# Kernel optimization log

Hardware: AMD Instinct MI355X
Metric: run time of the kernel (lower is better)

Reference implementation:

```python
import jax, jax.numpy as jnp
import numpy as np

TAU = 1.0
ALPHA = 1.0
BETA = 0.2  # note: torch module hardcodes self.beta = 0.2 regardless of the beta arg
EPS = 1e-10


def setup_inputs() -> dict:
    key = jax.random.key(0)
    k1, k2, k3 = jax.random.split(key, 3)
    N, H = 32768, 1024
    C, d, K = 8, 128, 512  # n_codebooks, code_size, K
    hidden_state = jax.random.normal(k1, (N, H), dtype=jnp.float32)
    codes = jax.random.normal(k2, (C, d, K), dtype=jnp.float32)
    u = jax.random.uniform(k3, (N, C, K), dtype=jnp.float32)
    gumbel = -jnp.log(-jnp.log(u + EPS) + EPS)  # standard Gumbel noise
    return {"hidden_state": hidden_state, "codes": codes, "gumbel": gumbel}


def reference(hidden_state, codes, gumbel):
    N, H = hidden_state.shape
    C, d, K = codes.shape
    h = hidden_state.reshape(N, C, d)  # codebook c owns columns [c*d, (c+1)*d)

    # cosine-similarity logits: (h @ code) / ||h|| / ||code||
    logits = jnp.einsum('ncd,cdk->nck', h, codes)
    feat_norms = jnp.linalg.norm(h, axis=2, keepdims=True)        # [N, C, 1]
    code_norms = jnp.linalg.norm(codes, axis=1)                   # [C, K]
    logits = logits / feat_norms / code_norms[None, :, :]

    # gumbel-softmax with hard=True (straight-through one-hot)
    y_soft = jax.nn.softmax((logits + gumbel) / TAU, axis=-1)     # [N, C, K]
    idx = jnp.argmax(y_soft, axis=-1)                             # [N, C]
    y_hard = jax.nn.one_hot(idx, K, dtype=y_soft.dtype)
    attention = y_hard + y_soft - jax.lax.stop_gradient(y_soft)

    # quantized hidden state
    nh = jnp.einsum('nck,cdk->ncd', attention, codes)             # [N, C, d]

    # VQ commitment / codebook losses (detach == stop_gradient)
    diff_commit = jax.lax.stop_gradient(nh) - h
    diff_code = nh - jax.lax.stop_gradient(h)
    loss = BETA * jnp.sum(jnp.linalg.norm(diff_commit, axis=2)) \
         + ALPHA * jnp.sum(jnp.linalg.norm(diff_code, axis=2))

    return nh.reshape(N, H), loss
```

## Files before the change

### kernel.cpp

```cpp
#include <hip/hip_runtime.h>
#include <hip/hip_bf16.h>
#include <stdint.h>

#define NROWS 32768
#define HDIM  1024
#define CNB   8
#define DCS   128
#define KCB   512
#define ROWS_PB 128

typedef short bf16x8 __attribute__((ext_vector_type(8)));
typedef float f32x4 __attribute__((ext_vector_type(4)));

__device__ __forceinline__ unsigned f2bfu(float x) {
  union { float f; unsigned u; } v; v.f = x;
  return (v.u + 0x7fffu + ((v.u >> 16) & 1u)) >> 16;
}
__device__ __forceinline__ float bfu2f(unsigned short b) {
  union { unsigned u; float f; } v; v.u = ((unsigned)b) << 16;
  return v.f;
}
__device__ __forceinline__ void gload_lds16(const void* g, void* l) {
  __builtin_amdgcn_global_load_lds(
      (const __attribute__((address_space(1))) uint32_t*)g,
      (__attribute__((address_space(3))) uint32_t*)l, 16, 0, 0);
}

__global__ __launch_bounds__(256) void prep_kernel(
    const float* __restrict__ codes, unsigned short* __restrict__ codesB,
    float* __restrict__ cn2, float* __restrict__ rcn, float* __restrict__ loss_slot) {
  const int c = blockIdx.y;
  const int k0 = blockIdx.x * 64;
  const int t = threadIdx.x;
  const int kl = t & 63;
  const int dq = t >> 6;
  const int k = k0 + kl;
  const float* src = codes + (size_t)c * DCS * KCB + k;
  char* dstbase = (char*)codesB + (size_t)c * 131072 + (size_t)(k >> 7) * 32768 + (k & 127) * 256;
  const unsigned swzk = (unsigned)(k & 7) << 4;
  float acc = 0.f;
#pragma unroll
  for (int g = 0; g < 4; ++g) {
    unsigned short pk[8];
#pragma unroll
    for (int j = 0; j < 8; ++j) {
      int d = dq * 32 + g * 8 + j;
      float v = src[(size_t)d * KCB];
      acc += v * v;
      pk[j] = (unsigned short)f2bfu(v);
    }
    unsigned d2 = (unsigned)((dq * 32 + g * 8) * 2);
    *(uint4*)(dstbase + (d2 ^ swzk)) = *(const uint4*)pk;
  }
  __shared__ float red[256];
  red[t] = acc;
  __syncthreads();
  if (t < 64) {
    float s = red[t] + red[t + 64] + red[t + 128] + red[t + 192];
    cn2[c * KCB + k0 + t] = s;
    rcn[c * KCB + k0 + t] = rsqrtf(s);
  }
  if (blockIdx.x == 0 && c == 0 && t == 0) *loss_slot = 0.f;
}

__global__ __launch_bounds__(512, 4) void vq_kernel(
    const float* __restrict__ hidden, const float* __restrict__ gumbel,
    const unsigned short* __restrict__ codesB, const float* __restrict__ cn2g,
    const float* __restrict__ rcn, float* __restrict__ out, float* __restrict__ loss_slot) {
  const int c = blockIdx.y;
  const int nb = blockIdx.x * ROWS_PB;
  const int tid = threadIdx.x;
  const int w = tid >> 6;
  const int l = tid & 63;
  const int l15 = l & 15;
  const int l4 = l >> 4;

  __shared__ char ldsB[32768];
  __shared__ float wloss[8];

  const char* cbase = (const char*)codesB + (size_t)c * 131072;

#pragma unroll
  for (int i = 0; i < 4; ++i)
    gload_lds16(cbase + i * 8192 + tid * 16, ldsB + i * 8192 + w * 1024);

  const int nrow = nb + w * 16 + l15;
  const float* hp = hidden + (size_t)nrow * HDIM + c * DCS + l4 * 8;
  float hv[4][8];
  float hn2 = 0.f;
#pragma unroll
  for (int s = 0; s < 4; ++s) {
    f32x4 p0 = *(const f32x4*)(hp + s * 32);
    f32x4 p1 = *(const f32x4*)(hp + s * 32 + 4);
#pragma unroll
    for (int j = 0; j < 4; ++j) { hv[s][j] = p0[j]; hv[s][4 + j] = p1[j]; }
#pragma unroll
    for (int j = 0; j < 8; ++j) hn2 += hv[s][j] * hv[s][j];
  }
  hn2 += __shfl_xor(hn2, 16);
  hn2 += __shfl_xor(hn2, 32);
  const float hnorm = sqrtf(hn2);
  const float rh = hnorm > 0.f ? 1.0f / hnorm : 0.f;
  bf16x8 afr[4];
#pragma unroll
  for (int s = 0; s < 4; ++s)
#pragma unroll
    for (int j = 0; j < 8; ++j) afr[s][j] = (short)f2bfu(hv[s][j] * rh);

  const float* gbase = gumbel + ((size_t)nrow * CNB + c) * KCB + l4 * 4;
  const float* rbase = rcn + c * KCB + l4 * 4;
  const unsigned swz = (unsigned)(l15 & 7) << 4;

  float bs = -3.4e38f, ba = 0.f;
  int bk = 0;

  __syncthreads();

#pragma unroll 1
  for (int kc = 0; kc < KCB; kc += 128) {
    f32x4 acc[8];
#pragma unroll
    for (int t = 0; t < 8; ++t) acc[t] = (f32x4){0.f, 0.f, 0.f, 0.f};
#pragma unroll
    for (int t = 0; t < 8; ++t) {
      const unsigned rowbase = (unsigned)((t * 16 + l15) * 256);
#pragma unroll
      for (int s = 0; s < 4; ++s) {
        bf16x8 bfr = *(const bf16x8*)(ldsB + rowbase + (((unsigned)(s * 64 + l4 * 16)) ^ swz));
        acc[t] = __builtin_amdgcn_mfma_f32_16x16x32_bf16(bfr, afr[s], acc[t], 0, 0, 0);
      }
    }
    __syncthreads();

    if (kc + 128 < KCB) {
      const char* src = cbase + (size_t)((kc >> 7) + 1) * 32768;
#pragma unroll
      for (int i = 0; i < 4; ++i)
        gload_lds16(src + i * 8192 + tid * 16, ldsB + i * 8192 + w * 1024);
    }

#pragma unroll
    for (int t = 0; t < 8; ++t) {
      f32x4 g = *(const f32x4*)(gbase + kc + t * 16);
      f32x4 rc = *(const f32x4*)(rbase + kc + t * 16);
#pragma unroll
      for (int r = 0; r < 4; ++r) {
        const int kf = kc + t * 16 + l4 * 4 + r;
        float sc = fmaf(acc[t][r], rc[r], g[r]);
        if (sc > bs) { bs = sc; bk = kf; ba = acc[t][r]; }
      }
    }
    __syncthreads();
  }

#pragma unroll
  for (int m = 16; m <= 32; m <<= 1) {
    float os = __shfl_xor(bs, m);
    int ok = __shfl_xor(bk, m);
    float oa = __shfl_xor(ba, m);
    if (os > bs || (os == bs && ok < bk)) { bs = os; bk = ok; ba = oa; }
  }

  const float c2 = cn2g[c * KCB + bk];
  const float arg = c2 + hn2 - 2.f * (ba * hnorm);
  float lsum = (l4 == 0) ? sqrtf(fmaxf(arg, 0.f)) : 0.f;

  const char* cb = cbase + (size_t)(bk >> 7) * 32768 + (bk & 127) * 256;
  const unsigned swzk = (unsigned)(bk & 7) << 4;
  float* op = out + (size_t)nrow * HDIM + c * DCS + l4 * 32;
#pragma unroll
  for (int j = 0; j < 4; ++j) {
    unsigned d2 = (unsigned)((l4 * 32 + j * 8) * 2);
    bf16x8 cv = *(const bf16x8*)(cb + (d2 ^ swzk));
    f32x4 o0, o1;
#pragma unroll
    for (int e = 0; e < 4; ++e) {
      o0[e] = bfu2f((unsigned short)cv[e]);
      o1[e] = bfu2f((unsigned short)cv[4 + e]);
    }
    *(f32x4*)(op + j * 8) = o0;
    *(f32x4*)(op + j * 8 + 4) = o1;
  }

#pragma unroll
  for (int m = 1; m <= 32; m <<= 1) lsum += __shfl_xor(lsum, m);
  if (l == 0) wloss[w] = lsum;
  __syncthreads();
  if (tid == 0) {
    float tot = 0.f;
#pragma unroll
    for (int i = 0; i < 8; ++i) tot += wloss[i];
    atomicAdd(loss_slot, tot * 1.2f);
  }
}

extern "C" void kernel_launch(void* const* d_in, const int* in_sizes, int n_in,
                              void* d_out, int out_size, void* d_ws, size_t ws_size,
                              hipStream_t stream) {
  const float* hidden = (const float*)d_in[0];
  const float* codes  = (const float*)d_in[1];
  const float* gumbel = (const float*)d_in[2];
  float* out = (float*)d_out;
  unsigned short* codesB = (unsigned short*)d_ws;
  float* cn2 = (float*)((char*)d_ws + (size_t)CNB * 131072);
  float* rcn = cn2 + CNB * KCB;
  float* loss_slot = out + (size_t)NROWS * HDIM;

  prep_kernel<<<dim3(8, CNB), 256, 0, stream>>>(codes, codesB, cn2, rcn, loss_slot);
  vq_kernel<<<dim3(NROWS / ROWS_PB, CNB), 512, 0, stream>>>(hidden, gumbel, codesB, cn2, rcn, out, loss_slot);
}
```

Before: 225.9 us.

## Double-buffer codebook LDS, prefetch gumbel, pre-normalize codes, nontemporal IO

Pre-normalizes codes to unit norm during prep, which removes the per-logit rcn load and multiply from the main loop. The output is rescaled by the code norm at write time. The codebook LDS buffer is doubled so two chunks are staged ahead and one barrier per chunk is removed, and gumbel loads for a chunk are issued before its MFMAs. Loads and stores use nontemporal hints. The cost is doubled LDS use (64KB per block), which may cut occupancy below the 4-block launch bound, plus a bf16 rounding change on the normalized codes and the rescaled output.

```diff
diff --git a/kernel.cpp b/kernel.cpp
--- a/kernel.cpp
+++ b/kernel.cpp
@@ -28,7 +28,7 @@
 
 __global__ __launch_bounds__(256) void prep_kernel(
     const float* __restrict__ codes, unsigned short* __restrict__ codesB,
-    float* __restrict__ cn2, float* __restrict__ rcn, float* __restrict__ loss_slot) {
+    float* __restrict__ cn2, float* __restrict__ loss_slot) {
   const int c = blockIdx.y;
   const int k0 = blockIdx.x * 64;
   const int t = threadIdx.x;
@@ -36,29 +36,30 @@
   const int dq = t >> 6;
   const int k = k0 + kl;
   const float* src = codes + (size_t)c * DCS * KCB + k;
-  char* dstbase = (char*)codesB + (size_t)c * 131072 + (size_t)(k >> 7) * 32768 + (k & 127) * 256;
-  const unsigned swzk = (unsigned)(k & 7) << 4;
+  float vbuf[32];
   float acc = 0.f;
 #pragma unroll
-  for (int g = 0; g < 4; ++g) {
-    unsigned short pk[8];
-#pragma unroll
-    for (int j = 0; j < 8; ++j) {
-      int d = dq * 32 + g * 8 + j;
-      float v = src[(size_t)d * KCB];
-      acc += v * v;
-      pk[j] = (unsigned short)f2bfu(v);
-    }
-    unsigned d2 = (unsigned)((dq * 32 + g * 8) * 2);
-    *(uint4*)(dstbase + (d2 ^ swzk)) = *(const uint4*)pk;
+  for (int i = 0; i < 32; ++i) {
+    float v = src[(size_t)(dq * 32 + i) * KCB];
+    vbuf[i] = v;
+    acc += v * v;
   }
   __shared__ float red[256];
   red[t] = acc;
   __syncthreads();
-  if (t < 64) {
-    float s = red[t] + red[t + 64] + red[t + 128] + red[t + 192];
-    cn2[c * KCB + k0 + t] = s;
-    rcn[c * KCB + k0 + t] = rsqrtf(s);
+  const float s = red[kl] + red[kl + 64] + red[kl + 128] + red[kl + 192];
+  const float rn = rsqrtf(s);
+  if (t < 64) cn2[c * KCB + k0 + t] = s;
+
+  char* dstbase = (char*)codesB + (size_t)c * 131072 + (size_t)(k >> 7) * 32768 + (k & 127) * 256;
+  const unsigned swzk = (unsigned)(k & 7) << 4;
+#pragma unroll
+  for (int g = 0; g < 4; ++g) {
+    unsigned short pk[8];
+#pragma unroll
+    for (int j = 0; j < 8; ++j) pk[j] = (unsigned short)f2bfu(vbuf[g * 8 + j] * rn);
+    unsigned d2 = (unsigned)((dq * 32 + g * 8) * 2);
+    *(uint4*)(dstbase + (d2 ^ swzk)) = *(const uint4*)pk;
   }
   if (blockIdx.x == 0 && c == 0 && t == 0) *loss_slot = 0.f;
 }
@@ -66,7 +67,7 @@
 __global__ __launch_bounds__(512, 4) void vq_kernel(
     const float* __restrict__ hidden, const float* __restrict__ gumbel,
     const unsigned short* __restrict__ codesB, const float* __restrict__ cn2g,
-    const float* __restrict__ rcn, float* __restrict__ out, float* __restrict__ loss_slot) {
+    float* __restrict__ out, float* __restrict__ loss_slot) {
   const int c = blockIdx.y;
   const int nb = blockIdx.x * ROWS_PB;
   const int tid = threadIdx.x;
@@ -75,28 +76,43 @@
   const int l15 = l & 15;
   const int l4 = l >> 4;
 
-  __shared__ char ldsB[32768];
+  __shared__ char ldsB[2 * 32768];
   __shared__ float wloss[8];
 
   const char* cbase = (const char*)codesB + (size_t)c * 131072;
 
-#pragma unroll
-  for (int i = 0; i < 4; ++i)
-    gload_lds16(cbase + i * 8192 + tid * 16, ldsB + i * 8192 + w * 1024);
+#define STAGE(chunk) { \
+    const char* _s = cbase + (size_t)(chunk) * 32768; \
+    char* _d = ldsB + ((chunk) & 1) * 32768 + w * 1024; \
+    gload_lds16(_s + 0 * 8192 + tid * 16, _d + 0 * 8192); \
+    gload_lds16(_s + 1 * 8192 + tid * 16, _d + 1 * 8192); \
+    gload_lds16(_s + 2 * 8192 + tid * 16, _d + 2 * 8192); \
+    gload_lds16(_s + 3 * 8192 + tid * 16, _d + 3 * 8192); }
 
   const int nrow = nb + w * 16 + l15;
   const float* hp = hidden + (size_t)nrow * HDIM + c * DCS + l4 * 8;
+  f32x4 hr[4][2];
+#pragma unroll
+  for (int s = 0; s < 4; ++s) {
+    hr[s][0] = __builtin_nontemporal_load((const f32x4*)(hp + s * 32));
+    hr[s][1] = __builtin_nontemporal_load((const f32x4*)(hp + s * 32 + 4));
+  }
+
+  STAGE(0)
+  STAGE(1)
+
+  float hn2 = 0.f;
   float hv[4][8];
-  float hn2 = 0.f;
-#pragma unroll
-  for (int s = 0; s < 4; ++s) {
-    f32x4 p0 = *(const f32x4*)(hp + s * 32);
-    f32x4 p1 = *(const f32x4*)(hp + s * 32 + 4);
-#pragma unroll
-    for (int j = 0; j < 4; ++j) { hv[s][j] = p0[j]; hv[s][4 + j] = p1[j]; }
+#pragma unroll
+  for (int s = 0; s < 4; ++s)
+#pragma unroll
+    for (int j = 0; j < 4; ++j) {
+      hv[s][j] = hr[s][0][j]; hv[s][4 + j] = hr[s][1][j];
+    }
+#pragma unroll
+  for (int s = 0; s < 4; ++s)
 #pragma unroll
     for (int j = 0; j < 8; ++j) hn2 += hv[s][j] * hv[s][j];
-  }
   hn2 += __shfl_xor(hn2, 16);
   hn2 += __shfl_xor(hn2, 32);
   const float hnorm = sqrtf(hn2);
@@ -108,7 +124,6 @@
     for (int j = 0; j < 8; ++j) afr[s][j] = (short)f2bfu(hv[s][j] * rh);
 
   const float* gbase = gumbel + ((size_t)nrow * CNB + c) * KCB + l4 * 4;
-  const float* rbase = rcn + c * KCB + l4 * 4;
   const unsigned swz = (unsigned)(l15 & 7) << 4;
 
   float bs = -3.4e38f, ba = 0.f;
@@ -116,8 +131,16 @@
 
   __syncthreads();
 
-#pragma unroll 1
-  for (int kc = 0; kc < KCB; kc += 128) {
+#pragma unroll
+  for (int i = 0; i < 4; ++i) {
+    const int kc = i * 128;
+    const char* buf = ldsB + (i & 1) * 32768;
+
+    f32x4 garr[8];
+#pragma unroll
+    for (int t = 0; t < 8; ++t)
+      garr[t] = __builtin_nontemporal_load((const f32x4*)(gbase + kc + t * 16));
+
     f32x4 acc[8];
 #pragma unroll
     for (int t = 0; t < 8; ++t) acc[t] = (f32x4){0.f, 0.f, 0.f, 0.f};
@@ -126,31 +149,23 @@
       const unsigned rowbase = (unsigned)((t * 16 + l15) * 256);
 #pragma unroll
       for (int s = 0; s < 4; ++s) {
-        bf16x8 bfr = *(const bf16x8*)(ldsB + rowbase + (((unsigned)(s * 64 + l4 * 16)) ^ swz));
+        bf16x8 bfr = *(const bf16x8*)(buf + rowbase + (((unsigned)(s * 64 + l4 * 16)) ^ swz));
         acc[t] = __builtin_amdgcn_mfma_f32_16x16x32_bf16(bfr, afr[s], acc[t], 0, 0, 0);
       }
     }
-    __syncthreads();
-
-    if (kc + 128 < KCB) {
-      const char* src = cbase + (size_t)((kc >> 7) + 1) * 32768;
-#pragma unroll
-      for (int i = 0; i < 4; ++i)
-        gload_lds16(src + i * 8192 + tid * 16, ldsB + i * 8192 + w * 1024);
-    }
 
 #pragma unroll
     for (int t = 0; t < 8; ++t) {
-      f32x4 g = *(const f32x4*)(gbase + kc + t * 16);
-      f32x4 rc = *(const f32x4*)(rbase + kc + t * 16);
 #pragma unroll
       for (int r = 0; r < 4; ++r) {
         const int kf = kc + t * 16 + l4 * 4 + r;
-        float sc = fmaf(acc[t][r], rc[r], g[r]);
+        float sc = acc[t][r] + garr[t][r];
         if (sc > bs) { bs = sc; bk = kf; ba = acc[t][r]; }
       }
     }
+
     __syncthreads();
+    if (i < 2) STAGE(i + 2)
   }
 
 #pragma unroll
@@ -162,7 +177,8 @@
   }
 
   const float c2 = cn2g[c * KCB + bk];
-  const float arg = c2 + hn2 - 2.f * (ba * hnorm);
+  const float cn = sqrtf(c2);
+  const float arg = c2 + hn2 - 2.f * (ba * hnorm * cn);
   float lsum = (l4 == 0) ? sqrtf(fmaxf(arg, 0.f)) : 0.f;
 
   const char* cb = cbase + (size_t)(bk >> 7) * 32768 + (bk & 127) * 256;
@@ -175,11 +191,11 @@
     f32x4 o0, o1;
 #pragma unroll
     for (int e = 0; e < 4; ++e) {
-      o0[e] = bfu2f((unsigned short)cv[e]);
-      o1[e] = bfu2f((unsigned short)cv[4 + e]);
-    }
-    *(f32x4*)(op + j * 8) = o0;
-    *(f32x4*)(op + j * 8 + 4) = o1;
+      o0[e] = bfu2f((unsigned short)cv[e]) * cn;
+      o1[e] = bfu2f((unsigned short)cv[4 + e]) * cn;
+    }
+    __builtin_nontemporal_store(o0, (f32x4*)(op + j * 8));
+    __builtin_nontemporal_store(o1, (f32x4*)(op + j * 8 + 4));
   }
 
 #pragma unroll
@@ -192,6 +208,7 @@
     for (int i = 0; i < 8; ++i) tot += wloss[i];
     atomicAdd(loss_slot, tot * 1.2f);
   }
+#undef STAGE
 }
 
 extern "C" void kernel_launch(void* const* d_in, const int* in_sizes, int n_in,
@@ -203,9 +220,8 @@
   float* out = (float*)d_out;
   unsigned short* codesB = (unsigned short*)d_ws;
   float* cn2 = (float*)((char*)d_ws + (size_t)CNB * 131072);
-  float* rcn = cn2 + CNB * KCB;
   float* loss_slot = out + (size_t)NROWS * HDIM;
 
-  prep_kernel<<<dim3(8, CNB), 256, 0, stream>>>(codes, codesB, cn2, rcn, loss_slot);
-  vq_kernel<<<dim3(NROWS / ROWS_PB, CNB), 512, 0, stream>>>(hidden, gumbel, codesB, cn2, rcn, out, loss_slot);
-}
+  prep_kernel<<<dim3(8, CNB), 256, 0, stream>>>(codes, codesB, cn2, loss_slot);
+  vq_kernel<<<dim3(NROWS / ROWS_PB, CNB), 512, 0, stream>>>(hidden, gumbel, codesB, cn2, out, loss_slot);
+}
```

Result: slower. 432.7 us (+91.5%).
